# Kernel optimization log

Hardware: AMD Instinct MI355X
Metric: run time of the kernel (lower is better)

Reference implementation:

```python
import jax, jax.numpy as jnp
import numpy as np

B, C, H, W = 8, 384, 32, 32
NUM_HEADS = 8
HEAD_DIM = C // NUM_HEADS


def setup_inputs() -> dict:
    key = jax.random.key(0)
    k1, k2, k3, k4, k5 = jax.random.split(key, 5)
    s = 1.0 / np.sqrt(C)
    return {
        "x": jax.random.normal(k1, (B, C, H, W), dtype=jnp.float32),
        "w_qkv": jax.random.normal(k2, (3 * C, C), dtype=jnp.float32) * s,   # 1x1 conv == linear over channels
        "b_qkv": jax.random.normal(k3, (3 * C,), dtype=jnp.float32) * 0.01,
        "w_proj": jax.random.normal(k4, (C, C), dtype=jnp.float32) * s,
        "b_proj": jax.random.normal(k5, (C,), dtype=jnp.float32) * 0.01,
    }


def reference(x, w_qkv, b_qkv, w_proj, b_proj):
    b, c, h, w = x.shape
    n = h * w
    scale = HEAD_DIM ** (-0.5)
    # 1x1 conv qkv: (B, 3C, H, W)
    qkv = jnp.einsum('bchw,oc->bohw', x, w_qkv) + b_qkv[None, :, None, None]
    # 'b (three hd d) h0 w0 -> three b hd (h0 w0) d'
    qkv = qkv.reshape(b, 3, NUM_HEADS, HEAD_DIM, n)
    qkv = jnp.transpose(qkv, (1, 0, 2, 4, 3))  # (3, B, heads, N, d)
    q, k, v = qkv[0], qkv[1], qkv[2]
    attn = jnp.einsum('bhnd,bhmd->bhnm', q, k) * scale
    attn = jax.nn.softmax(attn, axis=-1)
    out = jnp.einsum('bhnm,bhmd->bhnd', attn, v)          # (B, heads, N, d)
    out = jnp.transpose(out, (0, 1, 3, 2)).reshape(b, c, h, w)  # b (hd d) h w
    out = jnp.einsum('bchw,oc->bohw', out, w_proj) + b_proj[None, :, None, None]
    return out
```

## Files before the change

### kernel.cpp

```cpp
#include <hip/hip_runtime.h>
#include <hip/hip_bf16.h>

typedef __hip_bfloat16 bf16;
typedef __bf16 bfx8 __attribute__((ext_vector_type(8)));
typedef float f32x4 __attribute__((ext_vector_type(4)));

#define Bk   8
#define Ck   384
#define NHk  8
#define Dk   48
#define Dp   64
#define Nk   1024
#define O3   1152


__global__ __launch_bounds__(256) void prep_kernel(
    const float* __restrict__ x, const float* __restrict__ wq,
    const float* __restrict__ wp,
    bf16* __restrict__ Xs, bf16* __restrict__ Wq, bf16* __restrict__ Wp,
    bf16* __restrict__ Qs, bf16* __restrict__ Ks)
{
    __shared__ bf16 tile[32][33];
    const int bid = blockIdx.x;
    if (bid < 3072) {
        const int b = bid / 384, r = bid % 384;
        const int c0 = (r / 32) * 32, n0 = (r % 32) * 32;
        const int tn = threadIdx.x & 31, tc = threadIdx.x >> 5;
        const float* xb = x + (size_t)b * Ck * Nk;
        #pragma unroll
        for (int i = 0; i < 4; ++i)
            tile[tc + 8 * i][tn] = __float2bfloat16(xb[(size_t)(c0 + tc + 8 * i) * Nk + n0 + tn]);
        __syncthreads();
        bf16* base = Xs + ((size_t)b * 64 + (n0 >> 4)) * 48 * 128 + (c0 >> 3) * 128;
        #pragma unroll
        for (int i = 0; i < 4; ++i) {
            int n_loc = tc + 8 * i, c_loc = tn;
            base[(size_t)(n_loc >> 4) * 6144 + (c_loc >> 3) * 128 +
                 (n_loc & 15) * 8 + (c_loc & 7)] = tile[c_loc][n_loc];
        }
    } else {
        int i = (bid - 3072) * 256 + threadIdx.x;
        if (i < O3 * Ck) {
            int o = i / Ck, c = i - o * Ck;
            Wq[((size_t)(o >> 4) * 48 + (c >> 3)) * 128 + (o & 15) * 8 + (c & 7)] =
                __float2bfloat16(wq[i]);
        }
        if (i < Ck * Ck) {
            int o = i / Ck, c = i - o * Ck;
            Wp[((size_t)(o >> 4) * 48 + (c >> 3)) * 128 + (o & 15) * 8 + (c & 7)] =
                __float2bfloat16(wp[i]);
        }
        if (i < 262144) {
            int buf = i >> 17;
            int r17 = i & 131071;
            int head = r17 >> 11;
            int r11 = r17 & 2047;
            int g = r11 >> 5, c5 = r11 & 31;
            int cd = 6 + (c5 >> 4), e = c5 & 15;
            bf16* p = (buf ? Ks : Qs) + (size_t)head * 65536 +
                      ((size_t)g * 8 + cd) * 128 + e * 8;
            *(int4*)p = (int4){0, 0, 0, 0};
        }
    }
}

__global__ __launch_bounds__(256) void qkv_mfma_kernel(
    const bf16* __restrict__ Xs, const bf16* __restrict__ Wq,
    const float* __restrict__ bias,
    bf16* __restrict__ Qs, bf16* __restrict__ Ks, bf16* __restrict__ Vs)
{
    const int b    = blockIdx.z;
    const int by   = blockIdx.y;
    const int bx   = blockIdx.x;
    const int o0   = by * 64;
    const int n0   = bx * 128;
    const int wave = threadIdx.x >> 6;
    const int lane = threadIdx.x & 63;
    const int l15  = lane & 15, quad = lane >> 4;
    const int t3   = o0 / Ck;

    const bf16* xg[2];
    const bf16* wg[4];
    #pragma unroll
    for (int i = 0; i < 2; ++i)
        xg[i] = Xs + ((size_t)(b * 64 + bx * 8 + wave * 2 + i) * 48) * 128 + lane * 8;
    #pragma unroll
    for (int j = 0; j < 4; ++j)
        wg[j] = Wq + ((size_t)(by * 4 + j) * 48) * 128 + lane * 8;

    f32x4 acc[8];
    #pragma unroll
    for (int i = 0; i < 8; ++i) acc[i] = (f32x4){0.f, 0.f, 0.f, 0.f};

    if (t3 < 2) {
        #pragma unroll
        for (int s = 0; s < 12; ++s) {
            bfx8 fx[2], fw[4];
            #pragma unroll
            for (int i = 0; i < 2; ++i) fx[i] = *(const bfx8*)(xg[i] + s * 512);
            #pragma unroll
            for (int j = 0; j < 4; ++j) fw[j] = *(const bfx8*)(wg[j] + s * 512);
            #pragma unroll
            for (int i = 0; i < 2; ++i)
                #pragma unroll
                for (int j = 0; j < 4; ++j)
                    acc[i * 4 + j] = __builtin_amdgcn_mfma_f32_16x16x32_bf16(
                        fx[i], fw[j], acc[i * 4 + j], 0, 0, 0);
        }
        const float qscale = 0.2082350964f;
        #pragma unroll
        for (int j = 0; j < 4; ++j) {
            int o  = o0 + j * 16 + l15;
            float bi = bias[o];
            int r  = o - t3 * Ck;
            int hd = r / Dk, d = r - hd * Dk;
            bf16* hb = (t3 == 0 ? Qs : Ks) + (size_t)(b * NHk + hd) * 65536
                     + (d >> 3) * 128 + (d & 7);
            #pragma unroll
            for (int i = 0; i < 2; ++i) {
                #pragma unroll
                for (int reg = 0; reg < 4; ++reg) {
                    int npos = n0 + wave * 32 + i * 16 + quad * 4 + reg;
                    float v = acc[i * 4 + j][reg] + bi;
                    if (t3 == 0) v *= qscale;
                    hb[(size_t)(npos >> 4) * 1024 + (npos & 15) * 8] = __float2bfloat16(v);
                }
            }
        }
    } else {
        #pragma unroll
        for (int s = 0; s < 12; ++s) {
            bfx8 fx[2], fw[4];
            #pragma unroll
            for (int i = 0; i < 2; ++i) fx[i] = *(const bfx8*)(xg[i] + s * 512);
            #pragma unroll
            for (int j = 0; j < 4; ++j) fw[j] = *(const bfx8*)(wg[j] + s * 512);
            #pragma unroll
            for (int j = 0; j < 4; ++j)
                #pragma unroll
                for (int i = 0; i < 2; ++i)
                    acc[j * 2 + i] = __builtin_amdgcn_mfma_f32_16x16x32_bf16(
                        fw[j], fx[i], acc[j * 2 + i], 0, 0, 0);
        }
        #pragma unroll
        for (int j = 0; j < 4; ++j) {
            #pragma unroll
            for (int reg = 0; reg < 4; ++reg) {
                int o  = o0 + j * 16 + quad * 4 + reg;
                float bi = bias[o];
                int r  = o - 2 * Ck;
                int hd = r / Dk, d = r - hd * Dk;
                bf16* vb = Vs + (size_t)(b * NHk + hd) * 49152
                         + ((size_t)(d >> 4) * 128) * 128 + (d & 15) * 8;
                #pragma unroll
                for (int i = 0; i < 2; ++i) {
                    int npos = n0 + wave * 32 + i * 16 + l15;
                    vb[(size_t)(npos >> 3) * 128 + (npos & 7)] =
                        __float2bfloat16(acc[j * 2 + i][reg] + bi);
                }
            }
        }
    }
}

__global__ __launch_bounds__(256) void attn_kernel(
    const bf16* __restrict__ Qs, const bf16* __restrict__ Ks,
    const bf16* __restrict__ Vs, bf16* __restrict__ AO)
{
    __shared__ __align__(16) short Ps[4 * 16 * 72];
    __shared__ float sums[4][16];

    const int bx   = blockIdx.x;
    const int hd   = blockIdx.y;
    const int b    = blockIdx.z;
    const int t    = threadIdx.x;
    const int wave = t >> 6;
    const int lane = t & 63;
    const int l15  = lane & 15;
    const int quad = lane >> 4;
    const int grp  = bx * 4 + wave;

    const bf16* qb = Qs + (size_t)(b * NHk + hd) * 65536;
    const bf16* kb = Ks + (size_t)(b * NHk + hd) * 65536;
    const bf16* vb = Vs + (size_t)(b * NHk + hd) * 49152;

    const bf16* qp = qb + ((size_t)grp * 8 + quad) * 128 + l15 * 8;
    const bfx8 bq0 = *(const bfx8*)(qp);
    const bfx8 bq1 = *(const bfx8*)(qp + 512);

    float l_run = 0.f;
    f32x4 oacc[3];
    #pragma unroll
    for (int dc = 0; dc < 3; ++dc) oacc[dc] = (f32x4){0.f, 0.f, 0.f, 0.f};

    short* PsW = Ps + wave * 16 * 72;

    for (int k0 = 0; k0 < Nk; k0 += 64) {
        f32x4 sf[4];
        #pragma unroll
        for (int s = 0; s < 4; ++s) {
            const bf16* kp = kb + ((size_t)((k0 >> 4) + s) * 8 + quad) * 128 + l15 * 8;
            const bfx8 kf0 = *(const bfx8*)(kp);
            const bfx8 kf1 = *(const bfx8*)(kp + 512);
            f32x4 z = (f32x4){0.f, 0.f, 0.f, 0.f};
            z = __builtin_amdgcn_mfma_f32_16x16x32_bf16(kf0, bq0, z, 0, 0, 0);
            z = __builtin_amdgcn_mfma_f32_16x16x32_bf16(kf1, bq1, z, 0, 0, 0);
            sf[s] = z;
        }

        float lsum = 0.f;
        #pragma unroll
        for (int s = 0; s < 4; ++s) {
            ushort4 pk;
            float e0 = __builtin_amdgcn_exp2f(sf[s][0]);
            float e1 = __builtin_amdgcn_exp2f(sf[s][1]);
            float e2 = __builtin_amdgcn_exp2f(sf[s][2]);
            float e3 = __builtin_amdgcn_exp2f(sf[s][3]);
            lsum += (e0 + e1) + (e2 + e3);
            bf16 h0 = __float2bfloat16(e0), h1 = __float2bfloat16(e1);
            bf16 h2 = __float2bfloat16(e2), h3 = __float2bfloat16(e3);
            pk.x = *(unsigned short*)&h0; pk.y = *(unsigned short*)&h1;
            pk.z = *(unsigned short*)&h2; pk.w = *(unsigned short*)&h3;
            *(ushort4*)&PsW[l15 * 72 + s * 16 + quad * 4] = pk;
        }
        l_run += lsum;


        const bfx8 ap0 = *(const bfx8*)&PsW[l15 * 72 + quad * 8];
        const bfx8 ap1 = *(const bfx8*)&PsW[l15 * 72 + 32 + quad * 8];
        #pragma unroll
        for (int dc = 0; dc < 3; ++dc) {
            const bf16* vp = vb + ((size_t)dc * 128 + (k0 >> 3) + quad) * 128 + l15 * 8;
            const bfx8 bv0 = *(const bfx8*)(vp);
            const bfx8 bv1 = *(const bfx8*)(vp + 512);
            oacc[dc] = __builtin_amdgcn_mfma_f32_16x16x32_bf16(ap0, bv0, oacc[dc], 0, 0, 0);
            oacc[dc] = __builtin_amdgcn_mfma_f32_16x16x32_bf16(ap1, bv1, oacc[dc], 0, 0, 0);
        }
    }

    {
        float lt = l_run;
        lt += __shfl_xor(lt, 16, 64);
        lt += __shfl_xor(lt, 32, 64);
        sums[wave][l15] = lt;
    }

    short* OsW = PsW;
    #pragma unroll
    for (int r = 0; r < 4; ++r) {
        int qi = quad * 4 + r;
        float rli = 1.0f / sums[wave][qi];
        #pragma unroll
        for (int dcc = 0; dcc < 3; ++dcc) {
            bf16 hb = __float2bfloat16(oacc[dcc][r] * rli);
            OsW[qi * 64 + dcc * 16 + l15] = *(short*)&hb;
        }
    }

    bf16* aob = AO + (((size_t)b * 64 + grp) * 48 + hd * 6) * 128;
    {
        int u = lane;
        int4 v = *(const int4*)&OsW[(u & 15) * 64 + (u >> 4) * 8];
        *(int4*)(aob + u * 8) = v;
        if (lane < 32) {
            int u2 = 64 + lane;
            int4 v2 = *(const int4*)&OsW[(u2 & 15) * 64 + (u2 >> 4) * 8];
            *(int4*)(aob + u2 * 8) = v2;
        }
    }
}

__global__ __launch_bounds__(256) void proj_mfma_kernel(
    const bf16* __restrict__ AO, const bf16* __restrict__ Wp,
    const float* __restrict__ bias, float* __restrict__ out)
{
    const int b    = blockIdx.z;
    const int by   = blockIdx.y;
    const int bx   = blockIdx.x;
    const int o0   = by * 64;
    const int n0   = bx * 128;
    const int wave = threadIdx.x >> 6;
    const int lane = threadIdx.x & 63;
    const int l15  = lane & 15, quad = lane >> 4;

    const bf16* ag[2];
    const bf16* wg[4];
    #pragma unroll
    for (int i = 0; i < 2; ++i)
        ag[i] = AO + ((size_t)(b * 64 + bx * 8 + wave * 2 + i) * 48) * 128 + lane * 8;
    #pragma unroll
    for (int j = 0; j < 4; ++j)
        wg[j] = Wp + ((size_t)(by * 4 + j) * 48) * 128 + lane * 8;

    f32x4 acc[8];
    #pragma unroll
    for (int i = 0; i < 8; ++i) acc[i] = (f32x4){0.f, 0.f, 0.f, 0.f};

    #pragma unroll
    for (int s = 0; s < 12; ++s) {
        bfx8 fx[2], fw[4];
        #pragma unroll
        for (int i = 0; i < 2; ++i) fx[i] = *(const bfx8*)(ag[i] + s * 512);
        #pragma unroll
        for (int j = 0; j < 4; ++j) fw[j] = *(const bfx8*)(wg[j] + s * 512);
        #pragma unroll
        for (int j = 0; j < 4; ++j)
            #pragma unroll
            for (int i = 0; i < 2; ++i)
                acc[j * 2 + i] = __builtin_amdgcn_mfma_f32_16x16x32_bf16(
                    fw[j], fx[i], acc[j * 2 + i], 0, 0, 0);
    }

    #pragma unroll
    for (int j = 0; j < 4; ++j) {
        #pragma unroll
        for (int reg = 0; reg < 4; ++reg) {
            int o  = o0 + j * 16 + quad * 4 + reg;
            float bi = bias[o];
            #pragma unroll
            for (int i = 0; i < 2; ++i) {
                int npos = n0 + wave * 32 + i * 16 + l15;
                out[((size_t)b * Ck + o) * Nk + npos] = acc[j * 2 + i][reg] + bi;
            }
        }
    }
}

extern "C" void kernel_launch(void* const* d_in, const int* in_sizes, int n_in,
                              void* d_out, int out_size, void* d_ws, size_t ws_size,
                              hipStream_t stream)
{
    const float* x      = (const float*)d_in[0];
    const float* w_qkv  = (const float*)d_in[1];
    const float* b_qkv  = (const float*)d_in[2];
    const float* w_proj = (const float*)d_in[3];
    const float* b_proj = (const float*)d_in[4];
    float* out = (float*)d_out;

    const size_t XT_SEG = (size_t)Bk * Nk * Ck;
    const size_t WQ_SEG = (size_t)O3 * Ck;
    const size_t WP_SEG = (size_t)Ck * Ck;
    const size_t QK_SEG = (size_t)Bk * NHk * Nk * Dp;
    const size_t V_SEG  = (size_t)Bk * NHk * Dk * Nk;

    bf16* Xs = (bf16*)d_ws;
    bf16* Wq = Xs + XT_SEG;
    bf16* Wp = Wq + WQ_SEG;
    bf16* Qs = Wp + WP_SEG;
    bf16* Ks = Qs + QK_SEG;
    bf16* Vs = Ks + QK_SEG;
    bf16* AO = Vs + V_SEG;

    prep_kernel<<<4800, 256, 0, stream>>>(x, w_qkv, w_proj, Xs, Wq, Wp, Qs, Ks);
    qkv_mfma_kernel<<<dim3(Nk / 128, O3 / 64, Bk), 256, 0, stream>>>(
        Xs, Wq, b_qkv, Qs, Ks, Vs);
    attn_kernel<<<dim3(16, NHk, Bk), 256, 0, stream>>>(Qs, Ks, Vs, AO);
    proj_mfma_kernel<<<dim3(Nk / 128, Ck / 64, Bk), 256, 0, stream>>>(
        AO, Wp, b_proj, out);
}
```

Before: 134.6 us.

## Stage QKV epilogue through LDS for vectorized stores; double-buffer attention P tile

The QKV projection epilogue used to write scattered 2-byte bf16 values straight to global memory. It now writes them into a per-wave LDS tile and then emits coalesced 16-byte stores into the Q/K/V packed layouts. Separately, the attention loop is unrolled by two and alternates between two LDS P buffers, so consecutive tiles do not reuse the same scratch and the scheduler can overlap them. The cost is extra LDS in both kernels (about 20KB in the QKV kernel), which may lower occupancy, and in the attention kernel the per-wave P buffer is reused without an explicit barrier.

```diff
diff --git a/kernel.cpp b/kernel.cpp
--- a/kernel.cpp
+++ b/kernel.cpp
@@ -69,15 +69,18 @@
     const float* __restrict__ bias,
     bf16* __restrict__ Qs, bf16* __restrict__ Ks, bf16* __restrict__ Vs)
 {
+    __shared__ __align__(16) short T[4][2560];
+
     const int b    = blockIdx.z;
     const int by   = blockIdx.y;
     const int bx   = blockIdx.x;
     const int o0   = by * 64;
-    const int n0   = bx * 128;
     const int wave = threadIdx.x >> 6;
     const int lane = threadIdx.x & 63;
     const int l15  = lane & 15, quad = lane >> 4;
     const int t3   = o0 / Ck;
+
+    short* Tw = T[wave];
 
     const bf16* xg[2];
     const bf16* wg[4];
@@ -110,22 +113,30 @@
         const float qscale = 0.2082350964f;
         #pragma unroll
         for (int j = 0; j < 4; ++j) {
-            int o  = o0 + j * 16 + l15;
-            float bi = bias[o];
-            int r  = o - t3 * Ck;
-            int hd = r / Dk, d = r - hd * Dk;
-            bf16* hb = (t3 == 0 ? Qs : Ks) + (size_t)(b * NHk + hd) * 65536
-                     + (d >> 3) * 128 + (d & 7);
-            #pragma unroll
-            for (int i = 0; i < 2; ++i) {
+            float bi = bias[o0 + j * 16 + l15];
+            #pragma unroll
+            for (int i = 0; i < 2; ++i)
                 #pragma unroll
                 for (int reg = 0; reg < 4; ++reg) {
-                    int npos = n0 + wave * 32 + i * 16 + quad * 4 + reg;
                     float v = acc[i * 4 + j][reg] + bi;
                     if (t3 == 0) v *= qscale;
-                    hb[(size_t)(npos >> 4) * 1024 + (npos & 15) * 8] = __float2bfloat16(v);
+                    bf16 hb = __float2bfloat16(v);
+                    Tw[(i * 16 + quad * 4 + reg) * 72 + j * 16 + l15] = *(short*)&hb;
                 }
-            }
+        }
+        bf16* dstb = (t3 == 0 ? Qs : Ks);
+        #pragma unroll
+        for (int u = 0; u < 4; ++u) {
+            int idx = lane + 64 * u;
+            int oc = idx >> 5, r5 = idx & 31;
+            int ng = r5 >> 4, ni = r5 & 15;
+            int o = o0 + oc * 8;
+            int r = o - t3 * Ck;
+            int hd = r / Dk, dch = (r % Dk) >> 3;
+            int g = bx * 8 + wave * 2 + ng;
+            int4 v = *(const int4*)&Tw[(ng * 16 + ni) * 72 + oc * 8];
+            *(int4*)(dstb + (size_t)(b * NHk + hd) * 65536 +
+                     (size_t)g * 1024 + dch * 128 + ni * 8) = v;
         }
     } else {
         #pragma unroll
@@ -146,19 +157,26 @@
         for (int j = 0; j < 4; ++j) {
             #pragma unroll
             for (int reg = 0; reg < 4; ++reg) {
-                int o  = o0 + j * 16 + quad * 4 + reg;
-                float bi = bias[o];
-                int r  = o - 2 * Ck;
-                int hd = r / Dk, d = r - hd * Dk;
-                bf16* vb = Vs + (size_t)(b * NHk + hd) * 49152
-                         + ((size_t)(d >> 4) * 128) * 128 + (d & 15) * 8;
+                float bi = bias[o0 + j * 16 + quad * 4 + reg];
                 #pragma unroll
                 for (int i = 0; i < 2; ++i) {
-                    int npos = n0 + wave * 32 + i * 16 + l15;
-                    vb[(size_t)(npos >> 3) * 128 + (npos & 7)] =
-                        __float2bfloat16(acc[j * 2 + i][reg] + bi);
+                    bf16 hb = __float2bfloat16(acc[j * 2 + i][reg] + bi);
+                    Tw[(j * 16 + quad * 4 + reg) * 40 + i * 16 + l15] = *(short*)&hb;
                 }
             }
+        }
+        #pragma unroll
+        for (int u = 0; u < 4; ++u) {
+            int idx = lane + 64 * u;
+            int d_loc = idx >> 2, np8 = idx & 3;
+            int o = o0 + d_loc;
+            int r = o - 2 * Ck;
+            int hd = r / Dk, d = r % Dk;
+            int dg = d >> 4, din = d & 15;
+            int ng8 = bx * 16 + wave * 4 + np8;
+            int4 v = *(const int4*)&Tw[d_loc * 40 + np8 * 8];
+            *(int4*)(Vs + (size_t)(b * NHk + hd) * 49152 +
+                     ((size_t)dg * 128 + ng8) * 128 + din * 8) = v;
         }
     }
 }
@@ -167,7 +185,7 @@
     const bf16* __restrict__ Qs, const bf16* __restrict__ Ks,
     const bf16* __restrict__ Vs, bf16* __restrict__ AO)
 {
-    __shared__ __align__(16) short Ps[4 * 16 * 72];
+    __shared__ __align__(16) short Ps[2][4 * 16 * 72];
     __shared__ float sums[4][16];
 
     const int bx   = blockIdx.x;
@@ -193,9 +211,10 @@
     #pragma unroll
     for (int dc = 0; dc < 3; ++dc) oacc[dc] = (f32x4){0.f, 0.f, 0.f, 0.f};
 
-    short* PsW = Ps + wave * 16 * 72;
-
-    for (int k0 = 0; k0 < Nk; k0 += 64) {
+    short* PsW0 = Ps[0] + wave * 16 * 72;
+    short* PsW1 = Ps[1] + wave * 16 * 72;
+
+    auto tile = [&](int k0, short* PsW) {
         f32x4 sf[4];
         #pragma unroll
         for (int s = 0; s < 4; ++s) {
@@ -207,7 +226,6 @@
             z = __builtin_amdgcn_mfma_f32_16x16x32_bf16(kf1, bq1, z, 0, 0, 0);
             sf[s] = z;
         }
-
         float lsum = 0.f;
         #pragma unroll
         for (int s = 0; s < 4; ++s) {
@@ -225,7 +243,6 @@
         }
         l_run += lsum;
 
-
         const bfx8 ap0 = *(const bfx8*)&PsW[l15 * 72 + quad * 8];
         const bfx8 ap1 = *(const bfx8*)&PsW[l15 * 72 + 32 + quad * 8];
         #pragma unroll
@@ -236,6 +253,11 @@
             oacc[dc] = __builtin_amdgcn_mfma_f32_16x16x32_bf16(ap0, bv0, oacc[dc], 0, 0, 0);
             oacc[dc] = __builtin_amdgcn_mfma_f32_16x16x32_bf16(ap1, bv1, oacc[dc], 0, 0, 0);
         }
+    };
+
+    for (int kk = 0; kk < Nk; kk += 128) {
+        tile(kk, PsW0);
+        tile(kk + 64, PsW1);
     }
 
     {
@@ -245,7 +267,7 @@
         sums[wave][l15] = lt;
     }
 
-    short* OsW = PsW;
+    short* OsW = PsW0;
     #pragma unroll
     for (int r = 0; r < 4; ++r) {
         int qi = quad * 4 + r;
```

New measurement: 139.1 us. 3.4% more time.
